# Performance work log

Hardware: AMD Instinct MI355X
Metric: run time of the kernel (lower is better)

The kernel has to match this reference:

```python
import jax, jax.numpy as jnp
import numpy as np

T, I, H, L = 2048, 64, 512, 5  # seq len, input feat, hidden, layers


def _lstm_layer(x_seq, w_ih, w_hh, b_ih, b_hh):
    """Single-layer LSTM over time, batch=1. x_seq: [T, in]. Returns [T, H]."""
    n_hidden = w_hh.shape[1]
    b = b_ih + b_hh  # fuse biases once

    def step(carry, x_t):
        h, c = carry
        gates = w_ih @ x_t + w_hh @ h + b  # [4H]
        i, f, g, o = jnp.split(gates, 4)
        i = jax.nn.sigmoid(i)
        f = jax.nn.sigmoid(f)
        g = jnp.tanh(g)
        o = jax.nn.sigmoid(o)
        c = f * c + i * g
        h = o * jnp.tanh(c)
        return (h, c), h

    h0 = jnp.zeros((n_hidden,), x_seq.dtype)
    (_, _), hs = jax.lax.scan(step, (h0, h0), x_seq)
    return hs


def setup_inputs() -> dict:
    key = jax.random.key(0)
    ks = jax.random.split(key, 12)
    s = 1.0 / np.sqrt(H)  # PyTorch-style U(-1/sqrt(H), 1/sqrt(H)) scale, approximated with scaled normal
    return {
        "x": jax.random.normal(ks[0], (T, I), jnp.float32),
        "w_ih0": jax.random.normal(ks[1], (4 * H, I), jnp.float32) * s,
        "w_hh0": jax.random.normal(ks[2], (4 * H, H), jnp.float32) * s,
        "b_ih0": jax.random.normal(ks[3], (4 * H,), jnp.float32) * s,
        "b_hh0": jax.random.normal(ks[4], (4 * H,), jnp.float32) * s,
        "w_ih": jax.random.normal(ks[5], (L - 1, 4 * H, H), jnp.float32) * s,
        "w_hh": jax.random.normal(ks[6], (L - 1, 4 * H, H), jnp.float32) * s,
        "b_ih": jax.random.normal(ks[7], (L - 1, 4 * H), jnp.float32) * s,
        "b_hh": jax.random.normal(ks[8], (L - 1, 4 * H), jnp.float32) * s,
        "w_lin": jax.random.normal(ks[9], (1, H), jnp.float32) * s,
        "b_lin": jax.random.normal(ks[10], (1,), jnp.float32) * s,
    }


def reference(x, w_ih0, w_hh0, b_ih0, b_hh0, w_ih, w_hh, b_ih, b_hh, w_lin, b_lin):
    # 5-layer LSTM (dropout=0 / inference), batch = 1
    h = _lstm_layer(x, w_ih0, w_hh0, b_ih0, b_hh0)  # [T, H]
    for l in range(w_ih.shape[0]):  # fixed small layer loop
        h = _lstm_layer(h, w_ih[l], w_hh[l], b_ih[l], b_hh[l])
    e = h @ w_lin.T + b_lin                # [T, 1]
    w = jax.nn.softmax(jnp.tanh(e), axis=0)  # softmax over time
    res = jnp.mean(h * w, axis=0, keepdims=True)  # [1, H] (matches torch (T,1,H)*(T,1) mean over axis 0)
    return res
```

## Files before the change

### kernel.cpp

```cpp
#include <hip/hip_runtime.h>
#include <math.h>

#define TT 2048
#define II 64
#define HH 512
#define LL 5
#define RING 64
#define BPL 32
#define NBLK 256
#define WPB 16
#define SPIN_LIMIT 2000000L
#define BARRIER_SPIN 20000000L

typedef unsigned long long u64;
typedef unsigned u32;

__device__ __forceinline__ float wave_sum(float v) {
#pragma unroll
  for (int m = 32; m > 0; m >>= 1) v += __shfl_xor(v, m, 64);
  return v;
}

__device__ __forceinline__ float wave_max(float v) {
#pragma unroll
  for (int m = 32; m > 0; m >>= 1) v = fmaxf(v, __shfl_xor(v, m, 64));
  return v;
}

__device__ __forceinline__ float sigmoidf_(float v) {
  return 1.0f / (1.0f + expf(-v));
}

__device__ __forceinline__ u32 ld4(const u32* p) {
  return __hip_atomic_load((u32*)p, __ATOMIC_RELAXED, __HIP_MEMORY_SCOPE_AGENT);
}
__device__ __forceinline__ void st4(u32* p, u32 v) {
  __hip_atomic_store(p, v, __ATOMIC_RELAXED, __HIP_MEMORY_SCOPE_AGENT);
}
__device__ __forceinline__ u64 ld8(const u64* p) {
  return __hip_atomic_load((u64*)p, __ATOMIC_RELAXED, __HIP_MEMORY_SCOPE_AGENT);
}
__device__ __forceinline__ void st8(u64* p, u64 v) {
  __hip_atomic_store(p, v, __ATOMIC_RELAXED, __HIP_MEMORY_SCOPE_AGENT);
}

__device__ __forceinline__ float poll_ring(const u64* p, u32 want) {
  u64 a = ld8(p);
  u64 b = ld8(p);
  long sp = 0;
  while ((u32)(a >> 32) != want) {
    a = b;
    b = ld8(p);
    if (++sp > SPIN_LIMIT) { a = ((u64)want << 32); break; }
  }
  return __uint_as_float((u32)a);
}

__device__ __forceinline__ void wait_ge(u32* p, u32 v) {
  long spins = 0;
  while (ld4(p) < v) {
    if (++spins > BARRIER_SPIN) {
      __hip_atomic_fetch_max(p, v, __ATOMIC_RELAXED, __HIP_MEMORY_SCOPE_AGENT);
      break;
    }
  }
}

__device__ __forceinline__ void grid_barrier(u32* arrive, u32* gen, u32 idx) {
  __syncthreads();
  if (threadIdx.x == 0) {
    __threadfence();
    u32 target = (u32)NBLK * (idx + 1u);
    u32 prev = __hip_atomic_fetch_add(arrive, 1u, __ATOMIC_RELAXED, __HIP_MEMORY_SCOPE_AGENT);
    if (prev + 1u == target) {
      __hip_atomic_store(gen, idx + 1u, __ATOMIC_RELAXED, __HIP_MEMORY_SCOPE_AGENT);
    } else {
      wait_ge(gen, idx + 1u);
    }
    __threadfence();
  }
  __syncthreads();
}

extern "C" __global__ void __launch_bounds__(1024)
__attribute__((amdgpu_waves_per_eu(4, 4)))
lstm_pipe(
    const float* __restrict__ x,
    const float* __restrict__ w_ih0, const float* __restrict__ w_hh0,
    const float* __restrict__ b_ih0, const float* __restrict__ b_hh0,
    const float* __restrict__ w_ih, const float* __restrict__ w_hh,
    const float* __restrict__ b_ih, const float* __restrict__ b_hh,
    const float* __restrict__ w_lin, const float* __restrict__ b_lin,
    float* __restrict__ out, float* __restrict__ ws) {
  extern __shared__ float wihs[];
  __shared__ float hbuf[HH];
  __shared__ float xbuf[HH];
  __shared__ float sbuf[20];
  __shared__ int s_layer, s_slot;

  u32* cnt = (u32*)ws;
  u32* garr = cnt + 320;
  u32* ggen = cnt + 336;
  u32* claims = cnt + 352;
  u32* flagp = cnt + 448;

  u64* ring = (u64*)((char*)ws + 4096);
  float* h4 = (float*)(ring + (size_t)LL * RING * HH);
  float* h4T = h4 + (size_t)TT * HH;
  float* scores = h4T + (size_t)HH * TT;
  float* pbuf = scores + TT;
  float* red = pbuf + TT;

  const int b = blockIdx.x;
  const int tid = threadIdx.x;
  const int wv = tid >> 6;
  const int lane = tid & 63;

  if (tid == 0) {
    u32 xcc = 0;
    asm volatile("s_getreg_b32 %0, hwreg(HW_REG_XCC_ID)" : "=s"(xcc));
    xcc &= 7u;
    int layer = -1, slot = 0;
    if (xcc < LL) {
      u32 idx = __hip_atomic_fetch_add(claims + xcc * 16, 1u, __ATOMIC_RELAXED,
                                       __HIP_MEMORY_SCOPE_AGENT);
      if (idx < (u32)BPL) { layer = (int)xcc; slot = (int)idx; }
    }
    s_layer = layer; s_slot = slot;
  }
  grid_barrier(garr, ggen, 0u);
  if (b == 0 && tid == 0) {
    bool ok = true;
    for (int l = 0; l < LL; ++l) ok &= (ld4(claims + l * 16) >= (u32)BPL);
    st4(flagp, ok ? 1u : 2u);
  }
  grid_barrier(garr, ggen, 1u);
  if (tid == 0 && ld4(flagp) == 2u) {
    s_layer = (b < LL * BPL) ? (b / BPL) : -1;
    s_slot = (b < LL * BPL) ? (b % BPL) : 0;
  }
  __syncthreads();
  const int layer = s_layer;
  const int slot = s_slot;

  if (layer >= 0) {
    const int j = slot * WPB + wv;
    const bool is_last = (layer == LL - 1);
    u32* prog_l = cnt + layer * 64;
    u32* prog_lp1 = cnt + (layer + 1) * 64;
    u64* myring = ring + (size_t)layer * RING * HH;
    u64* prevring = ring + (size_t)(layer > 0 ? layer - 1 : 0) * RING * HH;

    float whh[4][8], bias[4];
    {
      const float* WHH = (layer == 0) ? w_hh0 : (w_hh + (size_t)(layer - 1) * 4 * HH * HH);
#pragma unroll
      for (int g = 0; g < 4; ++g) {
        const int row = g * HH + j;
#pragma unroll
        for (int m = 0; m < 8; ++m) whh[g][m] = WHH[(size_t)row * HH + m * 64 + lane];
      }
      if (layer == 0) {
#pragma unroll
        for (int g = 0; g < 4; ++g) bias[g] = b_ih0[g * HH + j] + b_hh0[g * HH + j];
      } else {
        const float* BIH = b_ih + (size_t)(layer - 1) * 4 * HH;
        const float* BHH = b_hh + (size_t)(layer - 1) * 4 * HH;
#pragma unroll
        for (int g = 0; g < 4; ++g) bias[g] = BIH[g * HH + j] + BHH[g * HH + j];
      }
      const float* WIH = (layer == 0) ? (const float*)0
                                      : (w_ih + (size_t)(layer - 1) * 4 * HH * HH);
      for (int f = tid; f < WPB * 4 * HH; f += 1024) {
        const int jj = f >> 11;
        const int g = (f >> 9) & 3;
        const int k = f & 511;
        const int row = g * HH + slot * WPB + jj;
        float v;
        if (layer == 0) v = (k < II) ? w_ih0[(size_t)row * II + k] : 0.0f;
        else v = WIH[(size_t)row * HH + k];
        wihs[f] = v;
      }
#pragma unroll
      for (int g = 0; g < 4; ++g) {
#pragma unroll
        for (int m = 0; m < 8; ++m) asm volatile("" : "+v"(whh[g][m]));
        asm volatile("" : "+v"(bias[g]));
      }
    }
    __syncthreads();

    float c = 0.0f;

    for (int t = 0; t < TT; ++t) {
      const int sl = t & (RING - 1);
      if (tid < HH) {
        if (t > 0) {
          hbuf[tid] =
              poll_ring(myring + (size_t)((t - 1) & (RING - 1)) * HH + tid, (u32)t);
        } else {
          hbuf[tid] = 0.0f;
        }
        if (tid == 0) {
          if (slot == 0 && t > 0 && (t & 3) == 0) st4(prog_l, (u32)t);
          if (layer < LL - 1 && t >= 64 && (t & 7) == 0) {
            long sp = 0;
            while (ld4(prog_lp1) < (u32)(t - 40) && ++sp < SPIN_LIMIT) {}
          }
        }
      } else {
        const int k = tid - HH;
        if (layer == 0) {
          xbuf[k] = (k < II) ? x[(size_t)t * II + k] : 0.0f;
        } else {
          xbuf[k] = poll_ring(prevring + (size_t)sl * HH + k, (u32)(t + 1));
        }
      }
      __syncthreads();

      float hp[8], xin[8];
#pragma unroll
      for (int m = 0; m < 8; ++m) {
        hp[m] = hbuf[m * 64 + lane];
        xin[m] = xbuf[m * 64 + lane];
      }
      float ai = 0.0f, af = 0.0f, ag = 0.0f, ao = 0.0f;
#pragma unroll
      for (int m = 0; m < 8; ++m) {
        ai = fmaf(whh[0][m], hp[m], ai);
        af = fmaf(whh[1][m], hp[m], af);
        ag = fmaf(whh[2][m], hp[m], ag);
        ao = fmaf(whh[3][m], hp[m], ao);
      }
      const float* wb = wihs + (size_t)wv * 4 * HH;
#pragma unroll
      for (int m = 0; m < 8; ++m) {
        const int o = m * 64 + lane;
        ai = fmaf(wb[0 * HH + o], xin[m], ai);
        af = fmaf(wb[1 * HH + o], xin[m], af);
        ag = fmaf(wb[2 * HH + o], xin[m], ag);
        ao = fmaf(wb[3 * HH + o], xin[m], ao);
      }
      ai = wave_sum(ai); af = wave_sum(af); ag = wave_sum(ag); ao = wave_sum(ao);
      float gi = sigmoidf_(ai + bias[0]);
      float gf = sigmoidf_(af + bias[1]);
      float gg = tanhf(ag + bias[2]);
      float go = sigmoidf_(ao + bias[3]);
      c = gf * c + gi * gg;
      float h = go * tanhf(c);

      if (lane == 0) {
        st8(myring + (size_t)sl * HH + j,
            (((u64)(u32)(t + 1)) << 32) | (u64)__float_as_uint(h));
        if (is_last) {
          h4[(size_t)t * HH + j] = h;
          h4T[(size_t)j * TT + t] = h;
        }
      }
      __syncthreads();
    }
  }

  grid_barrier(garr, ggen, 2u);

  {
    const int gw = b * WPB + wv;
    if (gw < TT) {
      const int t = gw;
      const float4* hp4 = (const float4*)(h4 + (size_t)t * HH + lane * 8);
      const float4* wl4 = (const float4*)(w_lin + lane * 8);
      float4 a = hp4[0], d = hp4[1], wa = wl4[0], wd = wl4[1];
      float acc = 0.0f;
      acc = fmaf(a.x, wa.x, acc); acc = fmaf(a.y, wa.y, acc);
      acc = fmaf(a.z, wa.z, acc); acc = fmaf(a.w, wa.w, acc);
      acc = fmaf(d.x, wd.x, acc); acc = fmaf(d.y, wd.y, acc);
      acc = fmaf(d.z, wd.z, acc); acc = fmaf(d.w, wd.w, acc);
      acc = wave_sum(acc);
      float sc = tanhf(acc + b_lin[0]);
      if (lane == 0) scores[t] = sc;
    }
  }
  grid_barrier(garr, ggen, 3u);

  if (b == 0) {
    float s0 = scores[tid];
    float s1 = scores[tid + 1024];
    float m = fmaxf(s0, s1);
    m = wave_max(m);
    if (lane == 0) sbuf[wv] = m;
    __syncthreads();
    if (tid == 0) {
      float M = sbuf[0];
      for (int k = 1; k < 16; ++k) M = fmaxf(M, sbuf[k]);
      sbuf[16] = M;
    }
    __syncthreads();
    float M = sbuf[16];
    float p0 = expf(s0 - M), p1 = expf(s1 - M);
    pbuf[tid] = p0;
    pbuf[tid + 1024] = p1;
    float ssum = wave_sum(p0 + p1);
    __syncthreads();
    if (lane == 0) sbuf[wv] = ssum;
    __syncthreads();
    if (tid == 0) {
      float S = 0.0f;
      for (int k = 0; k < 16; ++k) S += sbuf[k];
      red[0] = 1.0f / ((float)TT * S);
    }
  }
  grid_barrier(garr, ggen, 4u);

  {
    const int gw = b * WPB + wv;
    if (gw < HH) {
      const float scale = red[0];
      const float* hr = h4T + (size_t)gw * TT + lane * 32;
      const float* pr = pbuf + lane * 32;
      float acc = 0.0f;
#pragma unroll
      for (int m = 0; m < 32; ++m) acc = fmaf(hr[m], pr[m], acc);
      acc = wave_sum(acc);
      if (lane == 0) out[gw] = scale * acc;
    }
  }
}

extern "C" void kernel_launch(void* const* d_in, const int* in_sizes, int n_in,
                              void* d_out, int out_size, void* d_ws, size_t ws_size,
                              hipStream_t stream) {
  hipFuncSetAttribute((const void*)lstm_pipe,
                      hipFuncAttributeMaxDynamicSharedMemorySize, 131072);
  hipMemsetAsync(d_ws, 0, 4096, stream);
  lstm_pipe<<<dim3(NBLK), dim3(1024), 131072, stream>>>(
      (const float*)d_in[0],
      (const float*)d_in[1], (const float*)d_in[2],
      (const float*)d_in[3], (const float*)d_in[4],
      (const float*)d_in[5], (const float*)d_in[6],
      (const float*)d_in[7], (const float*)d_in[8],
      (const float*)d_in[9], (const float*)d_in[10],
      (float*)d_out, (float*)d_ws);
}
```

Before: 7.465 ms.

## Split each block into compute and loader waves with double-buffered step inputs

Each block now has 8 compute waves, each handling two hidden units with their recurrent weights held in registers. The other 8 waves act as loaders: they poll the rings for the next step's h and x and write them into double-buffered shared arrays, checking both rings together. This overlaps ring polling with gate computation and cuts the per-step block barriers from two to one. The cost is twice the register weight load per compute wave and half as many waves doing math, which lengthens the per-wave FMA and reduction chain.

```diff
diff --git a/kernel.cpp b/kernel.cpp
--- a/kernel.cpp
+++ b/kernel.cpp
@@ -8,7 +8,8 @@
 #define RING 64
 #define BPL 32
 #define NBLK 256
-#define WPB 16
+#define CW 8
+#define JPW 2
 #define SPIN_LIMIT 2000000L
 #define BARRIER_SPIN 20000000L
 
@@ -54,6 +55,25 @@
     if (++sp > SPIN_LIMIT) { a = ((u64)want << 32); break; }
   }
   return __uint_as_float((u32)a);
+}
+
+__device__ __forceinline__ void poll2(const u64* po, u32 wo, const u64* pp, u32 wp,
+                                      float* ro, float* rp) {
+  u64 va = ld8(po), vb = ld8(pp);
+  bool da = false, db = false;
+  long sp = 0;
+  for (;;) {
+    if (!da) {
+      if ((u32)(va >> 32) == wo) { *ro = __uint_as_float((u32)va); da = true; }
+      else va = ld8(po);
+    }
+    if (!db) {
+      if ((u32)(vb >> 32) == wp) { *rp = __uint_as_float((u32)vb); db = true; }
+      else vb = ld8(pp);
+    }
+    if (da && db) break;
+    if (++sp > SPIN_LIMIT) { if (!da) *ro = 0.0f; if (!db) *rp = 0.0f; break; }
+  }
 }
 
 __device__ __forceinline__ void wait_ge(u32* p, u32 v) {
@@ -93,8 +113,8 @@
     const float* __restrict__ w_lin, const float* __restrict__ b_lin,
     float* __restrict__ out, float* __restrict__ ws) {
   extern __shared__ float wihs[];
-  __shared__ float hbuf[HH];
-  __shared__ float xbuf[HH];
+  __shared__ float hbuf[2][HH];
+  __shared__ float xbuf[2][HH];
   __shared__ float sbuf[20];
   __shared__ int s_layer, s_slot;
 
@@ -144,127 +164,173 @@
   const int slot = s_slot;
 
   if (layer >= 0) {
-    const int j = slot * WPB + wv;
+    const bool is_comp = (wv < CW);
     const bool is_last = (layer == LL - 1);
+    const int j0 = slot * (CW * JPW) + wv * JPW;
     u32* prog_l = cnt + layer * 64;
     u32* prog_lp1 = cnt + (layer + 1) * 64;
     u64* myring = ring + (size_t)layer * RING * HH;
     u64* prevring = ring + (size_t)(layer > 0 ? layer - 1 : 0) * RING * HH;
 
-    float whh[4][8], bias[4];
-    {
+    float whh[JPW][4][8], bias[JPW][4];
+    if (is_comp) {
       const float* WHH = (layer == 0) ? w_hh0 : (w_hh + (size_t)(layer - 1) * 4 * HH * HH);
 #pragma unroll
-      for (int g = 0; g < 4; ++g) {
-        const int row = g * HH + j;
-#pragma unroll
-        for (int m = 0; m < 8; ++m) whh[g][m] = WHH[(size_t)row * HH + m * 64 + lane];
+      for (int jj = 0; jj < JPW; ++jj) {
+#pragma unroll
+        for (int g = 0; g < 4; ++g) {
+          const int row = g * HH + j0 + jj;
+#pragma unroll
+          for (int m = 0; m < 8; ++m)
+            whh[jj][g][m] = WHH[(size_t)row * HH + m * 64 + lane];
+        }
       }
       if (layer == 0) {
 #pragma unroll
-        for (int g = 0; g < 4; ++g) bias[g] = b_ih0[g * HH + j] + b_hh0[g * HH + j];
+        for (int jj = 0; jj < JPW; ++jj)
+#pragma unroll
+          for (int g = 0; g < 4; ++g)
+            bias[jj][g] = b_ih0[g * HH + j0 + jj] + b_hh0[g * HH + j0 + jj];
       } else {
         const float* BIH = b_ih + (size_t)(layer - 1) * 4 * HH;
         const float* BHH = b_hh + (size_t)(layer - 1) * 4 * HH;
 #pragma unroll
-        for (int g = 0; g < 4; ++g) bias[g] = BIH[g * HH + j] + BHH[g * HH + j];
+        for (int jj = 0; jj < JPW; ++jj)
+#pragma unroll
+          for (int g = 0; g < 4; ++g)
+            bias[jj][g] = BIH[g * HH + j0 + jj] + BHH[g * HH + j0 + jj];
       }
+#pragma unroll
+      for (int jj = 0; jj < JPW; ++jj) {
+#pragma unroll
+        for (int g = 0; g < 4; ++g) {
+#pragma unroll
+          for (int m = 0; m < 8; ++m) asm volatile("" : "+v"(whh[jj][g][m]));
+          asm volatile("" : "+v"(bias[jj][g]));
+        }
+      }
+    }
+    {
       const float* WIH = (layer == 0) ? (const float*)0
                                       : (w_ih + (size_t)(layer - 1) * 4 * HH * HH);
-      for (int f = tid; f < WPB * 4 * HH; f += 1024) {
-        const int jj = f >> 11;
+      for (int f = tid; f < 16 * 4 * HH; f += 1024) {
+        const int oo = f >> 11;
         const int g = (f >> 9) & 3;
         const int k = f & 511;
-        const int row = g * HH + slot * WPB + jj;
+        const int row = g * HH + slot * 16 + oo;
         float v;
         if (layer == 0) v = (k < II) ? w_ih0[(size_t)row * II + k] : 0.0f;
         else v = WIH[(size_t)row * HH + k];
         wihs[f] = v;
       }
-#pragma unroll
-      for (int g = 0; g < 4; ++g) {
-#pragma unroll
-        for (int m = 0; m < 8; ++m) asm volatile("" : "+v"(whh[g][m]));
-        asm volatile("" : "+v"(bias[g]));
-      }
+    }
+    if (!is_comp) {
+      const int k = tid - CW * 64;
+      hbuf[0][k] = 0.0f;
+      if (layer == 0) xbuf[0][k] = (k < II) ? x[k] : 0.0f;
+      else xbuf[0][k] = poll_ring(prevring + 0 * HH + k, 1u);
     }
     __syncthreads();
 
-    float c = 0.0f;
+    float c[JPW] = {0.0f, 0.0f};
 
     for (int t = 0; t < TT; ++t) {
-      const int sl = t & (RING - 1);
-      if (tid < HH) {
-        if (t > 0) {
-          hbuf[tid] =
-              poll_ring(myring + (size_t)((t - 1) & (RING - 1)) * HH + tid, (u32)t);
-        } else {
-          hbuf[tid] = 0.0f;
-        }
-        if (tid == 0) {
-          if (slot == 0 && t > 0 && (t & 3) == 0) st4(prog_l, (u32)t);
+      const int ph = t & 1;
+      if (is_comp) {
+        float hp[8], xin[8];
+#pragma unroll
+        for (int m = 0; m < 8; ++m) {
+          hp[m] = hbuf[ph][m * 64 + lane];
+          xin[m] = xbuf[ph][m * 64 + lane];
+        }
+        float acc[JPW][4];
+#pragma unroll
+        for (int jj = 0; jj < JPW; ++jj)
+#pragma unroll
+          for (int g = 0; g < 4; ++g) acc[jj][g] = 0.0f;
+#pragma unroll
+        for (int m = 0; m < 8; ++m) {
+          const float hv = hp[m];
+#pragma unroll
+          for (int jj = 0; jj < JPW; ++jj) {
+            acc[jj][0] = fmaf(whh[jj][0][m], hv, acc[jj][0]);
+            acc[jj][1] = fmaf(whh[jj][1][m], hv, acc[jj][1]);
+            acc[jj][2] = fmaf(whh[jj][2][m], hv, acc[jj][2]);
+            acc[jj][3] = fmaf(whh[jj][3][m], hv, acc[jj][3]);
+          }
+        }
+#pragma unroll
+        for (int m = 0; m < 8; ++m) {
+          const float xv = xin[m];
+          const int o = m * 64 + lane;
+#pragma unroll
+          for (int jj = 0; jj < JPW; ++jj) {
+            const float* wb = wihs + (size_t)(wv * JPW + jj) * 4 * HH;
+            acc[jj][0] = fmaf(wb[0 * HH + o], xv, acc[jj][0]);
+            acc[jj][1] = fmaf(wb[1 * HH + o], xv, acc[jj][1]);
+            acc[jj][2] = fmaf(wb[2 * HH + o], xv, acc[jj][2]);
+            acc[jj][3] = fmaf(wb[3 * HH + o], xv, acc[jj][3]);
+          }
+        }
+        float hout[JPW];
+#pragma unroll
+        for (int jj = 0; jj < JPW; ++jj) {
+          float ai = wave_sum(acc[jj][0]);
+          float af = wave_sum(acc[jj][1]);
+          float ag = wave_sum(acc[jj][2]);
+          float ao = wave_sum(acc[jj][3]);
+          float gi = sigmoidf_(ai + bias[jj][0]);
+          float gf = sigmoidf_(af + bias[jj][1]);
+          float gg = tanhf(ag + bias[jj][2]);
+          float go = sigmoidf_(ao + bias[jj][3]);
+          c[jj] = gf * c[jj] + gi * gg;
+          hout[jj] = go * tanhf(c[jj]);
+        }
+        if (lane == 0) {
+          const int sl = t & (RING - 1);
+          const u64 tg = ((u64)(u32)(t + 1)) << 32;
+          st8(myring + (size_t)sl * HH + j0, tg | (u64)__float_as_uint(hout[0]));
+          st8(myring + (size_t)sl * HH + j0 + 1, tg | (u64)__float_as_uint(hout[1]));
+          if (is_last) {
+            h4[(size_t)t * HH + j0] = hout[0];
+            h4[(size_t)t * HH + j0 + 1] = hout[1];
+            h4T[(size_t)j0 * TT + t] = hout[0];
+            h4T[(size_t)(j0 + 1) * TT + t] = hout[1];
+          }
+        }
+      } else {
+        const int k = tid - CW * 64;
+        if (t + 1 < TT) {
+          const int ph1 = ph ^ 1;
+          const int slo = t & (RING - 1);
+          const int slp = (t + 1) & (RING - 1);
+          if (layer == 0) {
+            xbuf[ph1][k] = (k < II) ? x[(size_t)(t + 1) * II + k] : 0.0f;
+            hbuf[ph1][k] = poll_ring(myring + (size_t)slo * HH + k, (u32)(t + 1));
+          } else {
+            float ro, rp;
+            poll2(myring + (size_t)slo * HH + k, (u32)(t + 1),
+                  prevring + (size_t)slp * HH + k, (u32)(t + 2), &ro, &rp);
+            hbuf[ph1][k] = ro;
+            xbuf[ph1][k] = rp;
+          }
+        }
+        if (k == 0) {
+          if (slot == 0 && (t & 3) == 0 && t > 0) st4(prog_l, (u32)t);
           if (layer < LL - 1 && t >= 64 && (t & 7) == 0) {
             long sp = 0;
             while (ld4(prog_lp1) < (u32)(t - 40) && ++sp < SPIN_LIMIT) {}
           }
         }
-      } else {
-        const int k = tid - HH;
-        if (layer == 0) {
-          xbuf[k] = (k < II) ? x[(size_t)t * II + k] : 0.0f;
-        } else {
-          xbuf[k] = poll_ring(prevring + (size_t)sl * HH + k, (u32)(t + 1));
-        }
       }
       __syncthreads();
-
-      float hp[8], xin[8];
-#pragma unroll
-      for (int m = 0; m < 8; ++m) {
-        hp[m] = hbuf[m * 64 + lane];
-        xin[m] = xbuf[m * 64 + lane];
-      }
-      float ai = 0.0f, af = 0.0f, ag = 0.0f, ao = 0.0f;
-#pragma unroll
-      for (int m = 0; m < 8; ++m) {
-        ai = fmaf(whh[0][m], hp[m], ai);
-        af = fmaf(whh[1][m], hp[m], af);
-        ag = fmaf(whh[2][m], hp[m], ag);
-        ao = fmaf(whh[3][m], hp[m], ao);
-      }
-      const float* wb = wihs + (size_t)wv * 4 * HH;
-#pragma unroll
-      for (int m = 0; m < 8; ++m) {
-        const int o = m * 64 + lane;
-        ai = fmaf(wb[0 * HH + o], xin[m], ai);
-        af = fmaf(wb[1 * HH + o], xin[m], af);
-        ag = fmaf(wb[2 * HH + o], xin[m], ag);
-        ao = fmaf(wb[3 * HH + o], xin[m], ao);
-      }
-      ai = wave_sum(ai); af = wave_sum(af); ag = wave_sum(ag); ao = wave_sum(ao);
-      float gi = sigmoidf_(ai + bias[0]);
-      float gf = sigmoidf_(af + bias[1]);
-      float gg = tanhf(ag + bias[2]);
-      float go = sigmoidf_(ao + bias[3]);
-      c = gf * c + gi * gg;
-      float h = go * tanhf(c);
-
-      if (lane == 0) {
-        st8(myring + (size_t)sl * HH + j,
-            (((u64)(u32)(t + 1)) << 32) | (u64)__float_as_uint(h));
-        if (is_last) {
-          h4[(size_t)t * HH + j] = h;
-          h4T[(size_t)j * TT + t] = h;
-        }
-      }
-      __syncthreads();
     }
   }
 
   grid_barrier(garr, ggen, 2u);
 
   {
-    const int gw = b * WPB + wv;
+    const int gw = b * 16 + wv;
     if (gw < TT) {
       const int t = gw;
       const float4* hp4 = (const float4*)(h4 + (size_t)t * HH + lane * 8);
@@ -312,7 +378,7 @@
   grid_barrier(garr, ggen, 4u);
 
   {
-    const int gw = b * WPB + wv;
+    const int gw = b * 16 + wv;
     if (gw < HH) {
       const float scale = red[0];
       const float* hr = h4T + (size_t)gw * TT + lane * 32;
```

After: 18.07 ms. 2.42x slower.

## Let each wave poll ring buffers directly and drop per-step block barriers

Applied to the files above, without the earlier changes.

Each wave now polls the recurrent and input ring buffers itself, pulling 8 values per lane straight into registers, instead of staging them through shared memory behind two __syncthreads per timestep. The input-weight shared-memory layout is interleaved by gate so one float4 load fetches all four gate weights. The backpressure wait on the next layer and the progress publish move to lane 0 of the individual waves. This removes block-wide synchronisation from the serial per-step critical path, at the cost of 16 times more global polling traffic per block and looser ordering of progress updates between waves.

```diff
diff --git a/kernel.cpp b/kernel.cpp
--- a/kernel.cpp
+++ b/kernel.cpp
@@ -44,16 +44,27 @@
   __hip_atomic_store(p, v, __ATOMIC_RELAXED, __HIP_MEMORY_SCOPE_AGENT);
 }
 
-__device__ __forceinline__ float poll_ring(const u64* p, u32 want) {
-  u64 a = ld8(p);
-  u64 b = ld8(p);
+__device__ __forceinline__ void poll8(const u64* base, u32 want, float* dst) {
+  u64 v[8];
+#pragma unroll
+  for (int m = 0; m < 8; ++m) v[m] = ld8(base + m * 64);
   long sp = 0;
-  while ((u32)(a >> 32) != want) {
-    a = b;
-    b = ld8(p);
-    if (++sp > SPIN_LIMIT) { a = ((u64)want << 32); break; }
-  }
-  return __uint_as_float((u32)a);
+  for (;;) {
+    bool ok = true;
+#pragma unroll
+    for (int m = 0; m < 8; ++m) {
+      if ((u32)(v[m] >> 32) != want) { ok = false; v[m] = ld8(base + m * 64); }
+    }
+    if (ok) break;
+    if (++sp > SPIN_LIMIT) {
+#pragma unroll
+      for (int m = 0; m < 8; ++m)
+        if ((u32)(v[m] >> 32) != want) v[m] = 0;
+      break;
+    }
+  }
+#pragma unroll
+  for (int m = 0; m < 8; ++m) dst[m] = __uint_as_float((u32)v[m]);
 }
 
 __device__ __forceinline__ void wait_ge(u32* p, u32 v) {
@@ -93,8 +104,6 @@
     const float* __restrict__ w_lin, const float* __restrict__ b_lin,
     float* __restrict__ out, float* __restrict__ ws) {
   extern __shared__ float wihs[];
-  __shared__ float hbuf[HH];
-  __shared__ float xbuf[HH];
   __shared__ float sbuf[20];
   __shared__ int s_layer, s_slot;
 
@@ -171,11 +180,13 @@
       }
       const float* WIH = (layer == 0) ? (const float*)0
                                       : (w_ih + (size_t)(layer - 1) * 4 * HH * HH);
-      for (int f = tid; f < WPB * 4 * HH; f += 1024) {
-        const int jj = f >> 11;
-        const int g = (f >> 9) & 3;
-        const int k = f & 511;
-        const int row = g * HH + slot * WPB + jj;
+      for (int f = tid; f < 16 * 8 * 64 * 4; f += 1024) {
+        const int g = f & 3;
+        const int ln = (f >> 2) & 63;
+        const int m = (f >> 8) & 7;
+        const int oo = f >> 11;
+        const int row = g * HH + slot * WPB + oo;
+        const int k = m * 64 + ln;
         float v;
         if (layer == 0) v = (k < II) ? w_ih0[(size_t)row * II + k] : 0.0f;
         else v = WIH[(size_t)row * HH + k];
@@ -194,36 +205,21 @@
 
     for (int t = 0; t < TT; ++t) {
       const int sl = t & (RING - 1);
-      if (tid < HH) {
-        if (t > 0) {
-          hbuf[tid] =
-              poll_ring(myring + (size_t)((t - 1) & (RING - 1)) * HH + tid, (u32)t);
-        } else {
-          hbuf[tid] = 0.0f;
-        }
-        if (tid == 0) {
-          if (slot == 0 && t > 0 && (t & 3) == 0) st4(prog_l, (u32)t);
-          if (layer < LL - 1 && t >= 64 && (t & 7) == 0) {
-            long sp = 0;
-            while (ld4(prog_lp1) < (u32)(t - 40) && ++sp < SPIN_LIMIT) {}
-          }
-        }
+      float hp[8], xin[8];
+      if (t > 0) {
+        poll8(myring + (size_t)((t - 1) & (RING - 1)) * HH + lane, (u32)t, hp);
       } else {
-        const int k = tid - HH;
-        if (layer == 0) {
-          xbuf[k] = (k < II) ? x[(size_t)t * II + k] : 0.0f;
-        } else {
-          xbuf[k] = poll_ring(prevring + (size_t)sl * HH + k, (u32)(t + 1));
-        }
-      }
-      __syncthreads();
-
-      float hp[8], xin[8];
-#pragma unroll
-      for (int m = 0; m < 8; ++m) {
-        hp[m] = hbuf[m * 64 + lane];
-        xin[m] = xbuf[m * 64 + lane];
-      }
+#pragma unroll
+        for (int m = 0; m < 8; ++m) hp[m] = 0.0f;
+      }
+      if (layer == 0) {
+        xin[0] = x[(size_t)t * II + lane];
+#pragma unroll
+        for (int m = 1; m < 8; ++m) xin[m] = 0.0f;
+      } else {
+        poll8(prevring + (size_t)sl * HH + lane, (u32)(t + 1), xin);
+      }
+
       float ai = 0.0f, af = 0.0f, ag = 0.0f, ao = 0.0f;
 #pragma unroll
       for (int m = 0; m < 8; ++m) {
@@ -232,14 +228,14 @@
         ag = fmaf(whh[2][m], hp[m], ag);
         ao = fmaf(whh[3][m], hp[m], ao);
       }
-      const float* wb = wihs + (size_t)wv * 4 * HH;
 #pragma unroll
       for (int m = 0; m < 8; ++m) {
-        const int o = m * 64 + lane;
-        ai = fmaf(wb[0 * HH + o], xin[m], ai);
-        af = fmaf(wb[1 * HH + o], xin[m], af);
-        ag = fmaf(wb[2 * HH + o], xin[m], ag);
-        ao = fmaf(wb[3 * HH + o], xin[m], ao);
+        const float4 w4 = *(const float4*)&wihs[(((size_t)wv * 8 + m) * 64 + lane) * 4];
+        const float xv = xin[m];
+        ai = fmaf(w4.x, xv, ai);
+        af = fmaf(w4.y, xv, af);
+        ag = fmaf(w4.z, xv, ag);
+        ao = fmaf(w4.w, xv, ao);
       }
       ai = wave_sum(ai); af = wave_sum(af); ag = wave_sum(ag); ao = wave_sum(ao);
       float gi = sigmoidf_(ai + bias[0]);
@@ -250,14 +246,18 @@
       float h = go * tanhf(c);
 
       if (lane == 0) {
+        if (layer < LL - 1 && t >= 64 && (t & 7) == 0) {
+          long sp = 0;
+          while (ld4(prog_lp1) < (u32)(t - 40) && ++sp < SPIN_LIMIT) {}
+        }
         st8(myring + (size_t)sl * HH + j,
             (((u64)(u32)(t + 1)) << 32) | (u64)__float_as_uint(h));
+        if (slot == 0 && wv == 0 && t > 0 && (t & 3) == 0) st4(prog_l, (u32)(t - 1));
         if (is_last) {
           h4[(size_t)t * HH + j] = h;
           h4T[(size_t)j * TT + t] = h;
         }
       }
-      __syncthreads();
     }
   }
 
```

New measurement: 22.40 ms. 200% more time.
